# Kernel optimization log

Measured on AMD Instinct MI355X. Metric: run time of the kernel, lower is better.

The kernel has to match this reference:

```python
import jax, jax.numpy as jnp
import numpy as np

B, T = 32, 4096
DIM_VECT, DIM_ATTN = 512, 256
DIM_ATTN_BID = 2 * DIM_ATTN  # flag_bid=True


def setup_inputs() -> dict:
    key = jax.random.key(0)
    k1, k2, k3, k4, k5, k6 = jax.random.split(key, 6)
    s = lambda fan_in: 1.0 / np.sqrt(fan_in)
    return {
        "vector": jax.random.normal(k1, (B, DIM_VECT), dtype=jnp.float32),
        "matrix": jax.random.normal(k2, (B, T, DIM_ATTN_BID), dtype=jnp.float32),
        "input_lengths": jax.random.randint(k3, (B,), 1, T + 1, dtype=jnp.int64),
        # nn.Linear weights are [out_features, in_features]
        "W_vec": jax.random.uniform(k4, (DIM_ATTN, DIM_VECT), jnp.float32, -s(DIM_VECT), s(DIM_VECT)),
        "W_mat": jax.random.uniform(k5, (DIM_ATTN, DIM_ATTN_BID), jnp.float32, -s(DIM_ATTN_BID), s(DIM_ATTN_BID)),
        "W_attn": jax.random.uniform(k6, (1, DIM_ATTN), jnp.float32, -s(DIM_ATTN), s(DIM_ATTN)),
    }


def reference(vector, matrix, input_lengths, W_vec, W_mat, W_attn):
    # vector: [B, Dv], matrix: [B, T, Dm], lengths: [B]
    t1 = jnp.einsum("bd,ad->ba", vector, W_vec)          # [B, A]
    t2 = jnp.einsum("btd,ad->bta", matrix, W_mat)        # [B, T, A]
    t3 = jax.nn.relu(t1[:, None, :] + t2)                # [B, T, A]
    logits = jnp.einsum("bta,oa->bt", t3, W_attn)        # [B, T] (o == 1 squeezed)
    # original subtracts the GLOBAL max over the whole logits tensor
    unnorm = jnp.exp(logits - logits.max())              # [B, T]
    mask = jnp.arange(matrix.shape[1])[None, :] < input_lengths[:, None]
    masked = unnorm * mask.astype(unnorm.dtype)
    attentions = masked / masked.sum(axis=1, keepdims=True)
    representations = jnp.einsum("btd,bt->bd", matrix, attentions)
    return representations, attentions
```

## Files before the change

kernel.cpp:

```cpp
#include <hip/hip_runtime.h>
#include <hip/hip_bf16.h>
#include <math.h>

#define B_SZ 32
#define T_SZ 4096
#define DV   512
#define DA   256
#define DK   512

typedef __attribute__((ext_vector_type(8))) __bf16 bf16x8;
typedef __attribute__((ext_vector_type(4))) __bf16 bf16x4;
typedef __attribute__((ext_vector_type(4))) float  f32x4;

__device__ inline int get_len(const int* __restrict__ p, int b) {
    return (p[1] == 0) ? p[2 * b] : p[b];
}

__global__ void conv_wmat_kernel(const float* __restrict__ w, __bf16* __restrict__ out) {
    int i = (blockIdx.x * 256 + threadIdx.x) * 4;
    float4 v = *(const float4*)(w + i);
    bf16x4 o;
    o[0] = (__bf16)v.x; o[1] = (__bf16)v.y; o[2] = (__bf16)v.z; o[3] = (__bf16)v.w;
    *(bf16x4*)(out + i) = o;
}

__global__ void t1_kernel(const float* __restrict__ vector, const float* __restrict__ wvec,
                          float* __restrict__ t1, float* __restrict__ rep) {
    int b = blockIdx.x, tid = threadIdx.x;
    __shared__ float sv[DV];
    sv[tid]       = vector[b * DV + tid];
    sv[tid + 256] = vector[b * DV + tid + 256];
    rep[b * DV + tid]       = 0.f;
    rep[b * DV + tid + 256] = 0.f;
    __syncthreads();
    const float4* w  = (const float4*)(wvec + (size_t)tid * DV);
    const float4* s4 = (const float4*)sv;
    float acc = 0.f;
#pragma unroll 8
    for (int k = 0; k < DV / 4; k++) {
        float4 wv = w[k]; float4 xv = s4[k];
        acc += wv.x * xv.x + wv.y * xv.y + wv.z * xv.z + wv.w * xv.w;
    }
    t1[b * DA + tid] = acc;
}

#define TM 64

__global__ __launch_bounds__(256) void logits_kernel(
    const float* __restrict__ matrix, const __bf16* __restrict__ wmat,
    const float* __restrict__ t1, const float* __restrict__ wattn,
    const int* __restrict__ lens, float* __restrict__ logits) {
    int b  = blockIdx.y;
    int t0 = blockIdx.x * TM;
    int len = get_len(lens, b);
    if (t0 >= len) return;

    __shared__ float s_t1[DA];
    __shared__ float s_wa[DA];
    __shared__ float s_logit[TM];

    int tid = threadIdx.x;
    s_t1[tid] = t1[b * DA + tid];
    s_wa[tid] = wattn[tid];
    if (tid < TM) s_logit[tid] = 0.f;
    __syncthreads();

    int wave = tid >> 6, lane = tid & 63;
    int col  = lane & 15;
    int koff = (lane >> 4) * 8;

    const float*  Arow[4];
    const __bf16* Brow[4];
#pragma unroll
    for (int mt = 0; mt < 4; mt++)
        Arow[mt] = matrix + ((size_t)b * T_SZ + t0 + mt * 16 + col) * DK + koff;
#pragma unroll
    for (int nt = 0; nt < 4; nt++)
        Brow[nt] = wmat + (size_t)(wave * 64 + nt * 16 + col) * DK + koff;

    f32x4 acc[4][4];
    f32x4 zero = {0.f, 0.f, 0.f, 0.f};
#pragma unroll
    for (int i = 0; i < 4; i++)
#pragma unroll
        for (int j = 0; j < 4; j++) acc[i][j] = zero;

    float4 a0[4], a1[4];
    uint4  bv[4];
#pragma unroll
    for (int mt = 0; mt < 4; mt++) {
        a0[mt] = *(const float4*)(Arow[mt]);
        a1[mt] = *(const float4*)(Arow[mt] + 4);
    }
#pragma unroll
    for (int nt = 0; nt < 4; nt++) bv[nt] = *(const uint4*)(Brow[nt]);

    for (int ks = 0; ks < DK / 32; ks++) {
        bf16x8 af[4], bfb[4];
#pragma unroll
        for (int mt = 0; mt < 4; mt++) {
            bf16x8 v;
            v[0] = (__bf16)a0[mt].x; v[1] = (__bf16)a0[mt].y;
            v[2] = (__bf16)a0[mt].z; v[3] = (__bf16)a0[mt].w;
            v[4] = (__bf16)a1[mt].x; v[5] = (__bf16)a1[mt].y;
            v[6] = (__bf16)a1[mt].z; v[7] = (__bf16)a1[mt].w;
            af[mt] = v;
        }
#pragma unroll
        for (int nt = 0; nt < 4; nt++) bfb[nt] = *(bf16x8*)&bv[nt];

        if (ks < DK / 32 - 1) {
            int k1 = (ks + 1) * 32;
#pragma unroll
            for (int mt = 0; mt < 4; mt++) {
                a0[mt] = *(const float4*)(Arow[mt] + k1);
                a1[mt] = *(const float4*)(Arow[mt] + k1 + 4);
            }
#pragma unroll
            for (int nt = 0; nt < 4; nt++) bv[nt] = *(const uint4*)(Brow[nt] + k1);
        }

#pragma unroll
        for (int mt = 0; mt < 4; mt++)
#pragma unroll
            for (int nt = 0; nt < 4; nt++)
                acc[mt][nt] = __builtin_amdgcn_mfma_f32_16x16x32_bf16(af[mt], bfb[nt], acc[mt][nt], 0, 0, 0);
    }

    int rg = lane >> 4;
#pragma unroll
    for (int mt = 0; mt < 4; mt++) {
#pragma unroll
        for (int r = 0; r < 4; r++) {
            float v = 0.f;
#pragma unroll
            for (int nt = 0; nt < 4; nt++) {
                int a = wave * 64 + nt * 16 + col;
                float x = acc[mt][nt][r] + s_t1[a];
                v += s_wa[a] * fmaxf(x, 0.f);
            }
#pragma unroll
            for (int off = 1; off < 16; off <<= 1) v += __shfl_xor(v, off, 64);
            if (col == 0) atomicAdd(&s_logit[mt * 16 + rg * 4 + r], v);
        }
    }
    __syncthreads();
    if (tid < TM) logits[(size_t)b * T_SZ + t0 + tid] = s_logit[tid];
}

__global__ __launch_bounds__(1024) void softmax_kernel(const int* __restrict__ lens,
                                                       float* __restrict__ attn) {
    int b = blockIdx.x, tid = threadIdx.x;
    int len = get_len(lens, b);
    float* row = attn + (size_t)b * T_SZ;
    __shared__ float sred[16];

    float r[4];
#pragma unroll
    for (int i = 0; i < 4; i++) r[i] = row[tid + i * 1024];

    float m = -1e30f;
#pragma unroll
    for (int i = 0; i < 4; i++)
        if (tid + i * 1024 < len) m = fmaxf(m, r[i]);
#pragma unroll
    for (int off = 32; off; off >>= 1) m = fmaxf(m, __shfl_xor(m, off, 64));
    if ((tid & 63) == 0) sred[tid >> 6] = m;
    __syncthreads();
    m = sred[0];
#pragma unroll
    for (int i = 1; i < 16; i++) m = fmaxf(m, sred[i]);
    __syncthreads();

    float e[4];
    float s = 0.f;
#pragma unroll
    for (int i = 0; i < 4; i++) {
        e[i] = (tid + i * 1024 < len) ? __expf(r[i] - m) : 0.f;
        s += e[i];
    }
#pragma unroll
    for (int off = 32; off; off >>= 1) s += __shfl_xor(s, off, 64);
    if ((tid & 63) == 0) sred[tid >> 6] = s;
    __syncthreads();
    s = 0.f;
#pragma unroll
    for (int i = 0; i < 16; i++) s += sred[i];
    float inv = 1.f / s;

#pragma unroll
    for (int i = 0; i < 4; i++) row[tid + i * 1024] = e[i] * inv;
}

#define TC 128
__global__ void rep_kernel(const float* __restrict__ matrix, const float* __restrict__ attn,
                           const int* __restrict__ lens, float* __restrict__ rep) {
    int b = blockIdx.y, c = blockIdx.x, tid = threadIdx.x;
    int len = get_len(lens, b);
    int t0 = c * TC;
    if (t0 >= len) return;
    __shared__ float sa[TC];
    if (tid < TC) sa[tid] = attn[(size_t)b * T_SZ + t0 + tid];
    __syncthreads();
    int n = min(TC, len - t0);
    const float* M = matrix + ((size_t)b * T_SZ + t0) * DK;
    float ax = 0.f, ay = 0.f;
    int d = 2 * tid;
#pragma unroll 8
    for (int t = 0; t < n; t++) {
        float w = sa[t];
        float2 mv = *(const float2*)(M + (size_t)t * DK + d);
        ax = fmaf(w, mv.x, ax);
        ay = fmaf(w, mv.y, ay);
    }
    atomicAdd(&rep[b * DV + d], ax);
    atomicAdd(&rep[b * DV + d + 1], ay);
}

extern "C" void kernel_launch(void* const* d_in, const int* in_sizes, int n_in,
                              void* d_out, int out_size, void* d_ws, size_t ws_size,
                              hipStream_t stream) {
    const float* vector = (const float*)d_in[0];
    const float* matrix = (const float*)d_in[1];
    const int*   lens   = (const int*)d_in[2];
    const float* wvec   = (const float*)d_in[3];
    const float* wmat   = (const float*)d_in[4];
    const float* wattn  = (const float*)d_in[5];

    float* rep  = (float*)d_out;
    float* attn = rep + B_SZ * DV;

    float*  t1      = (float*)d_ws;
    __bf16* wmat_bf = (__bf16*)((char*)d_ws + 32768);

    conv_wmat_kernel<<<dim3((DA * DK) / (256 * 4)), 256, 0, stream>>>(wmat, wmat_bf);
    t1_kernel<<<dim3(B_SZ), 256, 0, stream>>>(vector, wvec, t1, rep);
    logits_kernel<<<dim3(T_SZ / TM, B_SZ), 256, 0, stream>>>(matrix, wmat_bf, t1, wattn, lens, attn);
    softmax_kernel<<<dim3(B_SZ), 1024, 0, stream>>>(lens, attn);
    rep_kernel<<<dim3(T_SZ / TC, B_SZ), 256, 0, stream>>>(matrix, attn, lens, rep);
}
```

Measured before the change: 475.9 us.

## Stage matrix tiles through double-buffered LDS, merge setup kernels, widen rep loads

The logits kernel now loads the fp32 matrix tile with coalesced row-contiguous float4 loads, converts it to bf16 into a double-buffered padded LDS tile, and reads MFMA fragments from LDS with a 64-wide K step. Previously each lane read strided row fragments straight from global memory. The weight conversion and t1 kernels are merged into one launch to save a launch. The rep kernel switches to float4 loads, with the token range split across two halves of the block. The cost is extra LDS traffic and a barrier on every K step.

```diff
diff --git a/kernel.cpp b/kernel.cpp
--- a/kernel.cpp
+++ b/kernel.cpp
@@ -16,17 +16,19 @@
     return (p[1] == 0) ? p[2 * b] : p[b];
 }
 
-__global__ void conv_wmat_kernel(const float* __restrict__ w, __bf16* __restrict__ out) {
-    int i = (blockIdx.x * 256 + threadIdx.x) * 4;
-    float4 v = *(const float4*)(w + i);
-    bf16x4 o;
-    o[0] = (__bf16)v.x; o[1] = (__bf16)v.y; o[2] = (__bf16)v.z; o[3] = (__bf16)v.w;
-    *(bf16x4*)(out + i) = o;
-}
-
-__global__ void t1_kernel(const float* __restrict__ vector, const float* __restrict__ wvec,
-                          float* __restrict__ t1, float* __restrict__ rep) {
-    int b = blockIdx.x, tid = threadIdx.x;
+__global__ void setup_kernel(const float* __restrict__ wmat, __bf16* __restrict__ wmat_bf,
+                             const float* __restrict__ vector, const float* __restrict__ wvec,
+                             float* __restrict__ t1, float* __restrict__ rep) {
+    int blk = blockIdx.x, tid = threadIdx.x;
+    if (blk < 128) {
+        int i = (blk * 256 + tid) * 4;
+        float4 v = *(const float4*)(wmat + i);
+        bf16x4 o;
+        o[0] = (__bf16)v.x; o[1] = (__bf16)v.y; o[2] = (__bf16)v.z; o[3] = (__bf16)v.w;
+        *(bf16x4*)(wmat_bf + i) = o;
+        return;
+    }
+    int b = blk - 128;
     __shared__ float sv[DV];
     sv[tid]       = vector[b * DV + tid];
     sv[tid + 256] = vector[b * DV + tid + 256];
@@ -44,7 +46,8 @@
     t1[b * DA + tid] = acc;
 }
 
-#define TM 64
+#define TM  64
+#define LDA 72
 
 __global__ __launch_bounds__(256) void logits_kernel(
     const float* __restrict__ matrix, const __bf16* __restrict__ wmat,
@@ -55,6 +58,7 @@
     int len = get_len(lens, b);
     if (t0 >= len) return;
 
+    __shared__ __bf16 sA[2][TM][LDA];
     __shared__ float s_t1[DA];
     __shared__ float s_wa[DA];
     __shared__ float s_logit[TM];
@@ -63,20 +67,19 @@
     s_t1[tid] = t1[b * DA + tid];
     s_wa[tid] = wattn[tid];
     if (tid < TM) s_logit[tid] = 0.f;
-    __syncthreads();
 
     int wave = tid >> 6, lane = tid & 63;
     int col  = lane & 15;
     int koff = (lane >> 4) * 8;
 
-    const float*  Arow[4];
-    const __bf16* Brow[4];
-#pragma unroll
-    for (int mt = 0; mt < 4; mt++)
-        Arow[mt] = matrix + ((size_t)b * T_SZ + t0 + mt * 16 + col) * DK + koff;
+    int srow = tid >> 4;
+    int soff = (tid & 15) * 4;
+
+    const float* Abase = matrix + ((size_t)b * T_SZ + t0) * DK;
+    const __bf16* Bp[4];
 #pragma unroll
     for (int nt = 0; nt < 4; nt++)
-        Brow[nt] = wmat + (size_t)(wave * 64 + nt * 16 + col) * DK + koff;
+        Bp[nt] = wmat + (size_t)(wave * 64 + nt * 16 + col) * DK + koff;
 
     f32x4 acc[4][4];
     f32x4 zero = {0.f, 0.f, 0.f, 0.f};
@@ -85,46 +88,65 @@
 #pragma unroll
         for (int j = 0; j < 4; j++) acc[i][j] = zero;
 
-    float4 a0[4], a1[4];
-    uint4  bv[4];
-#pragma unroll
-    for (int mt = 0; mt < 4; mt++) {
-        a0[mt] = *(const float4*)(Arow[mt]);
-        a1[mt] = *(const float4*)(Arow[mt] + 4);
-    }
-#pragma unroll
-    for (int nt = 0; nt < 4; nt++) bv[nt] = *(const uint4*)(Brow[nt]);
-
-    for (int ks = 0; ks < DK / 32; ks++) {
-        bf16x8 af[4], bfb[4];
-#pragma unroll
-        for (int mt = 0; mt < 4; mt++) {
-            bf16x8 v;
-            v[0] = (__bf16)a0[mt].x; v[1] = (__bf16)a0[mt].y;
-            v[2] = (__bf16)a0[mt].z; v[3] = (__bf16)a0[mt].w;
-            v[4] = (__bf16)a1[mt].x; v[5] = (__bf16)a1[mt].y;
-            v[6] = (__bf16)a1[mt].z; v[7] = (__bf16)a1[mt].w;
-            af[mt] = v;
-        }
-#pragma unroll
-        for (int nt = 0; nt < 4; nt++) bfb[nt] = *(bf16x8*)&bv[nt];
-
-        if (ks < DK / 32 - 1) {
-            int k1 = (ks + 1) * 32;
-#pragma unroll
-            for (int mt = 0; mt < 4; mt++) {
-                a0[mt] = *(const float4*)(Arow[mt] + k1);
-                a1[mt] = *(const float4*)(Arow[mt] + k1 + 4);
+    {
+#pragma unroll
+        for (int r = 0; r < 4; r++) {
+            float4 v = *(const float4*)(Abase + (size_t)(srow + r * 16) * DK + soff);
+            bf16x4 o;
+            o[0] = (__bf16)v.x; o[1] = (__bf16)v.y; o[2] = (__bf16)v.z; o[3] = (__bf16)v.w;
+            *(bf16x4*)&sA[0][srow + r * 16][soff] = o;
+        }
+    }
+    uint4 pb[8];
+#pragma unroll
+    for (int s = 0; s < 2; s++)
+#pragma unroll
+        for (int nt = 0; nt < 4; nt++)
+            pb[s * 4 + nt] = *(const uint4*)(Bp[nt] + s * 32);
+
+    __syncthreads();
+
+    for (int ks = 0; ks < 8; ks++) {
+        int buf = ks & 1;
+        float4 na[4];
+        uint4  nb[8];
+        if (ks < 7) {
+            int k1 = (ks + 1) * 64;
+#pragma unroll
+            for (int r = 0; r < 4; r++)
+                na[r] = *(const float4*)(Abase + (size_t)(srow + r * 16) * DK + k1 + soff);
+#pragma unroll
+            for (int s = 0; s < 2; s++)
+#pragma unroll
+                for (int nt = 0; nt < 4; nt++)
+                    nb[s * 4 + nt] = *(const uint4*)(Bp[nt] + k1 + s * 32);
+        }
+        bf16x8 af[2][4];
+#pragma unroll
+        for (int s = 0; s < 2; s++)
+#pragma unroll
+            for (int mt = 0; mt < 4; mt++)
+                af[s][mt] = *(const bf16x8*)&sA[buf][mt * 16 + col][s * 32 + koff];
+#pragma unroll
+        for (int s = 0; s < 2; s++)
+#pragma unroll
+            for (int mt = 0; mt < 4; mt++)
+#pragma unroll
+                for (int nt = 0; nt < 4; nt++)
+                    acc[mt][nt] = __builtin_amdgcn_mfma_f32_16x16x32_bf16(
+                        af[s][mt], *(bf16x8*)&pb[s * 4 + nt], acc[mt][nt], 0, 0, 0);
+        if (ks < 7) {
+#pragma unroll
+            for (int r = 0; r < 4; r++) {
+                bf16x4 o;
+                o[0] = (__bf16)na[r].x; o[1] = (__bf16)na[r].y;
+                o[2] = (__bf16)na[r].z; o[3] = (__bf16)na[r].w;
+                *(bf16x4*)&sA[buf ^ 1][srow + r * 16][soff] = o;
             }
 #pragma unroll
-            for (int nt = 0; nt < 4; nt++) bv[nt] = *(const uint4*)(Brow[nt] + k1);
-        }
-
-#pragma unroll
-        for (int mt = 0; mt < 4; mt++)
-#pragma unroll
-            for (int nt = 0; nt < 4; nt++)
-                acc[mt][nt] = __builtin_amdgcn_mfma_f32_16x16x32_bf16(af[mt], bfb[nt], acc[mt][nt], 0, 0, 0);
+            for (int i = 0; i < 8; i++) pb[i] = nb[i];
+        }
+        __syncthreads();
     }
 
     int rg = lane >> 4;
@@ -203,18 +225,25 @@
     if (tid < TC) sa[tid] = attn[(size_t)b * T_SZ + t0 + tid];
     __syncthreads();
     int n = min(TC, len - t0);
+    int half = tid >> 7;
+    int l = tid & 127;
+    int d = l * 4;
+    int nh = (n + 1) >> 1;
+    int tb = half ? nh : 0;
+    int te = half ? n : nh;
     const float* M = matrix + ((size_t)b * T_SZ + t0) * DK;
-    float ax = 0.f, ay = 0.f;
-    int d = 2 * tid;
-#pragma unroll 8
-    for (int t = 0; t < n; t++) {
+    float a0 = 0.f, a1 = 0.f, a2 = 0.f, a3 = 0.f;
+#pragma unroll 4
+    for (int t = tb; t < te; t++) {
         float w = sa[t];
-        float2 mv = *(const float2*)(M + (size_t)t * DK + d);
-        ax = fmaf(w, mv.x, ax);
-        ay = fmaf(w, mv.y, ay);
-    }
-    atomicAdd(&rep[b * DV + d], ax);
-    atomicAdd(&rep[b * DV + d + 1], ay);
+        float4 mv = *(const float4*)(M + (size_t)t * DK + d);
+        a0 = fmaf(w, mv.x, a0); a1 = fmaf(w, mv.y, a1);
+        a2 = fmaf(w, mv.z, a2); a3 = fmaf(w, mv.w, a3);
+    }
+    atomicAdd(&rep[b * DV + d],     a0);
+    atomicAdd(&rep[b * DV + d + 1], a1);
+    atomicAdd(&rep[b * DV + d + 2], a2);
+    atomicAdd(&rep[b * DV + d + 3], a3);
 }
 
 extern "C" void kernel_launch(void* const* d_in, const int* in_sizes, int n_in,
@@ -233,8 +262,7 @@
     float*  t1      = (float*)d_ws;
     __bf16* wmat_bf = (__bf16*)((char*)d_ws + 32768);
 
-    conv_wmat_kernel<<<dim3((DA * DK) / (256 * 4)), 256, 0, stream>>>(wmat, wmat_bf);
-    t1_kernel<<<dim3(B_SZ), 256, 0, stream>>>(vector, wvec, t1, rep);
+    setup_kernel<<<dim3(160), 256, 0, stream>>>(wmat, wmat_bf, vector, wvec, t1, rep);
     logits_kernel<<<dim3(T_SZ / TM, B_SZ), 256, 0, stream>>>(matrix, wmat_bf, t1, wattn, lens, attn);
     softmax_kernel<<<dim3(B_SZ), 1024, 0, stream>>>(lens, attn);
     rep_kernel<<<dim3(T_SZ / TC, B_SZ), 256, 0, stream>>>(matrix, attn, lens, rep);
```

New measurement: 416.9 us. 1.14x faster.
